# Performance work log

Measured on AMD Instinct MI355X. Metric: run time of the kernel, lower is better.

The kernel has to match this reference:

```python
import jax, jax.numpy as jnp
import numpy as np

N_NODES = 50000
N_EDGES = 500000
IN_CH = 128
HID = 32
HEADS = 4
OUT_CH = 64
NEG_SLOPE = 0.2


def setup_inputs() -> dict:
    key = jax.random.key(0)
    ks = jax.random.split(key, 12)
    s = 0.1  # weight init scale
    x = jax.random.normal(ks[0], (N_NODES, IN_CH), jnp.float32)
    edge_index = jax.random.randint(ks[1], (2, N_EDGES), 0, N_NODES)
    # conv1: GATv2Conv(IN_CH, HID, heads=HEADS)
    W1l = jax.random.normal(ks[2], (IN_CH, HEADS * HID), jnp.float32) * s  # lin_l (source)
    W1r = jax.random.normal(ks[3], (IN_CH, HEADS * HID), jnp.float32) * s  # lin_r (target)
    att1 = jax.random.normal(ks[4], (HEADS, HID), jnp.float32) * s
    b1 = jnp.zeros((HEADS * HID,), jnp.float32)
    # conv2: GATv2Conv(HEADS*HID, OUT_CH, heads=1, concat=False)
    W2l = jax.random.normal(ks[5], (HEADS * HID, OUT_CH), jnp.float32) * s
    W2r = jax.random.normal(ks[6], (HEADS * HID, OUT_CH), jnp.float32) * s
    att2 = jax.random.normal(ks[7], (1, OUT_CH), jnp.float32) * s
    b2 = jnp.zeros((OUT_CH,), jnp.float32)
    return {"x": x, "edge_index": edge_index, "W1l": W1l, "W1r": W1r,
            "att1": att1, "b1": b1, "W2l": W2l, "W2r": W2r, "att2": att2, "b2": b2}


def gatv2_conv(x, src, dst, Wl, Wr, att, heads, ch, num_nodes):
    """GATv2Conv message passing. Returns [N, heads, ch] (pre-bias, pre-concat)."""
    xl = (x @ Wl).reshape(num_nodes, heads, ch)  # source transform
    xr = (x @ Wr).reshape(num_nodes, heads, ch)  # target transform
    xl_e = xl[src]                               # [E, H, C] gathered source feats
    m = jax.nn.leaky_relu(xl_e + xr[dst], NEG_SLOPE)
    score = jnp.einsum('ehc,hc->eh', m, att)     # [E, H]
    # segment softmax over incoming edges per destination node
    smax = jax.ops.segment_max(score, dst, num_segments=num_nodes)
    smax = jnp.where(jnp.isfinite(smax), smax, 0.0)
    p = jnp.exp(score - smax[dst])
    denom = jax.ops.segment_sum(p, dst, num_segments=num_nodes)
    alpha = p / (denom[dst] + 1e-16)
    out = jax.ops.segment_sum(alpha[:, :, None] * xl_e, dst, num_segments=num_nodes)
    return out


def reference(x, edge_index, W1l, W1r, att1, b1, W2l, W2r, att2, b2):
    n = x.shape[0]
    loop = jnp.arange(n, dtype=edge_index.dtype)
    src = jnp.concatenate([edge_index[0], loop])  # add self-loops (PyG default)
    dst = jnp.concatenate([edge_index[1], loop])
    # dropout(p=0.6) is identity in eval mode
    h = gatv2_conv(x, src, dst, W1l, W1r, att1, HEADS, HID, n)
    h = h.reshape(n, HEADS * HID) + b1            # concat=True
    h = jax.nn.elu(h)
    o = gatv2_conv(h, src, dst, W2l, W2r, att2, 1, OUT_CH, n)  # [N, 1, OUT]
    o = o + b2                                     # concat=False, heads=1 -> mean == identity
    return o[:, 0, :]
```

## Files before the change

kernel.cpp:

```cpp
#include <hip/hip_runtime.h>
#include <hip/hip_bf16.h>
#include <math.h>

#define N_NODESC 50000
#define N_EDGESC 500000
#define E_TOT    (N_EDGESC + N_NODESC)
#define IN_CH 128
#define HID 32
#define HEADS 4
#define HC (HEADS*HID)
#define OUT_CH 64
#define NEG_SLOPE 0.2f
#define NB_SCAN 196
#define N_STRIPS (N_NODESC/16)

typedef unsigned short u16;
typedef __attribute__((ext_vector_type(8))) short short8;
typedef __attribute__((ext_vector_type(4))) float floatx4;

__device__ __forceinline__ u16 f2bf(float f){
  unsigned u = __float_as_uint(f);
  return (u16)((u + 0x7FFFu + ((u >> 16) & 1u)) >> 16);
}
__device__ __forceinline__ float bf2f(u16 b){ return __uint_as_float(((unsigned)b) << 16); }
__device__ __forceinline__ float bflo(unsigned q){ return __uint_as_float(q << 16); }
__device__ __forceinline__ float bfhi(unsigned q){ return __uint_as_float(q & 0xFFFF0000u); }
__device__ __forceinline__ float lrelu(float v){ return (v > 0.f) ? v : NEG_SLOPE*v; }

__device__ __forceinline__ void edge_sd(const int* __restrict__ ei, int e, int& s, int& d){
  if (e < N_EDGESC){ s = ei[e]; d = ei[N_EDGESC + e]; }
  else { s = e - N_EDGESC; d = s; }
}

__global__ void k_zero_deg(int* __restrict__ deg){
  int i = blockIdx.x*blockDim.x + threadIdx.x;
  if (i < N_NODESC) deg[i] = 0;
}

__global__ void k_hist(const int* __restrict__ ei, int* __restrict__ deg){
  int e = blockIdx.x*blockDim.x + threadIdx.x;
  if (e >= E_TOT) return;
  int s, d; edge_sd(ei, e, s, d);
  atomicAdd(&deg[d], 1);
}

__global__ void k_scan_a(const int* __restrict__ deg, int* __restrict__ rs,
                         int* __restrict__ bsum){
  __shared__ int sh[256];
  int i = blockIdx.x*256 + threadIdx.x;
  int v = (i < N_NODESC) ? deg[i] : 0;
  sh[threadIdx.x] = v;
  __syncthreads();
  for (int off=1; off<256; off<<=1){
    int t = (threadIdx.x >= off) ? sh[threadIdx.x-off] : 0;
    __syncthreads();
    sh[threadIdx.x] += t;
    __syncthreads();
  }
  if (i < N_NODESC) rs[i] = sh[threadIdx.x] - v;
  if (threadIdx.x == 255) bsum[blockIdx.x] = sh[255];
}

__global__ void k_scan_b(int* __restrict__ bsum){
  __shared__ int sh[256];
  int v = (threadIdx.x < NB_SCAN) ? bsum[threadIdx.x] : 0;
  sh[threadIdx.x] = v;
  __syncthreads();
  for (int off=1; off<256; off<<=1){
    int t = (threadIdx.x >= off) ? sh[threadIdx.x-off] : 0;
    __syncthreads();
    sh[threadIdx.x] += t;
    __syncthreads();
  }
  if (threadIdx.x < NB_SCAN) bsum[threadIdx.x] = sh[threadIdx.x] - v;
}

__global__ void k_scan_c(int* __restrict__ rs, const int* __restrict__ bsum,
                         int* __restrict__ cursor){
  int i = blockIdx.x*256 + threadIdx.x;
  if (i >= N_NODESC) return;
  int v = rs[i] + bsum[blockIdx.x];
  rs[i] = v;
  cursor[i] = v;
}

__global__ void k_fill(const int* __restrict__ ei, int* __restrict__ cursor,
                       int* __restrict__ csrc){
  int e = blockIdx.x*blockDim.x + threadIdx.x;
  if (e >= E_TOT) return;
  int s, d; edge_sd(ei, e, s, d);
  int pos = atomicAdd(&cursor[d], 1);
  csrc[pos] = s;
}

__global__ void k_split(const float* __restrict__ X, u16* __restrict__ hi,
                        u16* __restrict__ lo, int total4){
  int i = blockIdx.x*blockDim.x + threadIdx.x;
  if (i >= total4) return;
  float4 v = ((const float4*)X)[i];
  ushort4 h, l;
  h.x = f2bf(v.x); l.x = f2bf(v.x - bf2f(h.x));
  h.y = f2bf(v.y); l.y = f2bf(v.y - bf2f(h.y));
  h.z = f2bf(v.z); l.z = f2bf(v.z - bf2f(h.z));
  h.w = f2bf(v.w); l.w = f2bf(v.w - bf2f(h.w));
  ((ushort4*)hi)[i] = h;
  ((ushort4*)lo)[i] = l;
}

__global__ void k_prep_all(const float* __restrict__ W1l, const float* __restrict__ W1r,
                           const float* __restrict__ W2l, const float* __restrict__ W2r,
                           u16* __restrict__ w1lh, u16* __restrict__ w1rh,
                           u16* __restrict__ w2lh, u16* __restrict__ w2rh){
  int b = blockIdx.x;
  const float* W; u16 *Th; int N, base;
  if (b < 8)      { W=W1l; Th=w1lh; N=HC;     base=b;    }
  else if (b < 16){ W=W1r; Th=w1rh; N=HC;     base=b-8;  }
  else if (b < 20){ W=W2l; Th=w2lh; N=OUT_CH; base=b-16; }
  else            { W=W2r; Th=w2rh; N=OUT_CH; base=b-20; }
  int tid = base*256 + threadIdx.x;
  int lane = tid & 63;
  int t = (tid >> 6) & 3;
  int c = tid >> 8;
  int k0 = t*32 + (lane>>4)*8;
  int n  = c*16 + (lane&15);
  #pragma unroll
  for (int j=0;j<8;j++){
    Th[(size_t)tid*8 + j] = f2bf(W[(size_t)(k0+j)*N + n]);
  }
}

template<int NCW, int SPB>
__launch_bounds__(256, 2)
__global__ void k_gemm_regB(const u16* __restrict__ Ahi, const u16* __restrict__ Alo,
                            const u16* __restrict__ BlT, const u16* __restrict__ BrT,
                            u16* __restrict__ Olb, float* __restrict__ Or){
  constexpr int NLD = 2*NCW*16;
  int wave = threadIdx.x >> 6, lane = threadIdx.x & 63;
  int m = lane & 15, quad = lane >> 4;
  bool isl = (wave < 2);
  int ctbase = (isl ? wave : wave - 2) * NCW;
  const u16* __restrict__ BT = isl ? BlT : BrT;

  short8 breg[NCW][4];
  #pragma unroll
  for (int c=0;c<NCW;c++)
    #pragma unroll
    for (int t=0;t<4;t++)
      breg[c][t] = *(const short8*)(BT + ((size_t)(((ctbase+c)*4 + t)*64) + lane)*8);

  int strip0 = blockIdx.x * SPB;
  short8 ah[2][4], al[2][4];

  {
    const u16* p1 = Ahi + (size_t)(strip0*16 + m)*128 + quad*8;
    const u16* p2 = Alo + (size_t)(strip0*16 + m)*128 + quad*8;
    #pragma unroll
    for (int t=0;t<4;t++){
      ah[0][t] = *(const short8*)(p1 + t*32);
      al[0][t] = *(const short8*)(p2 + t*32);
    }
  }

  #pragma unroll
  for (int i=0;i<SPB;i++){
    int s = strip0 + i;
    if (s >= N_STRIPS) break;
    if (i+1 < SPB && s+1 < N_STRIPS){
      const u16* p1 = Ahi + (size_t)((s+1)*16 + m)*128 + quad*8;
      const u16* p2 = Alo + (size_t)((s+1)*16 + m)*128 + quad*8;
      #pragma unroll
      for (int t=0;t<4;t++){
        ah[(i+1)&1][t] = *(const short8*)(p1 + t*32);
        al[(i+1)&1][t] = *(const short8*)(p2 + t*32);
      }
    }
    const int b = i&1;
    floatx4 acc[NCW];
    #pragma unroll
    for (int c=0;c<NCW;c++) acc[c] = (floatx4){0.f,0.f,0.f,0.f};
    #pragma unroll
    for (int t=0;t<4;t++){
      #pragma unroll
      for (int c=0;c<NCW;c++){
        acc[c] = __builtin_amdgcn_mfma_f32_16x16x32_bf16(ah[b][t], breg[c][t], acc[c], 0,0,0);
        acc[c] = __builtin_amdgcn_mfma_f32_16x16x32_bf16(al[b][t], breg[c][t], acc[c], 0,0,0);
      }
    }
    int row0 = s*16;
    if (isl){
      #pragma unroll
      for (int c=0;c<NCW;c++)
        #pragma unroll
        for (int r=0;r<4;r++)
          Olb[(size_t)(row0 + quad*4 + r)*NLD + (ctbase+c)*16 + m] = f2bf(acc[c][r]);
    } else {
      #pragma unroll
      for (int c=0;c<NCW;c++)
        #pragma unroll
        for (int r=0;r<4;r++)
          Or[(size_t)(row0 + quad*4 + r)*NLD + (ctbase+c)*16 + m] = acc[c][r];
    }
  }
}

__global__ void k_fused1(const int* __restrict__ rs, const int* __restrict__ deg,
                         const int* __restrict__ csrc, const u16* __restrict__ xlb,
                         const float* __restrict__ xr, const float* __restrict__ att,
                         const float* __restrict__ b1,
                         u16* __restrict__ Hhi, u16* __restrict__ Hlo){
  int wave = threadIdx.x >> 6;
  int lane = threadIdx.x & 63;
  int d = blockIdx.x*4 + wave;
  if (d >= N_NODESC) return;

  float2 xrv = ((const float2*)(xr + (size_t)d*HC))[lane];
  float2 atv = ((const float2*)att)[lane];
  float2 bv  = ((const float2*)b1)[lane];

  int start = rs[d];
  int degd  = deg[d];
  const unsigned* __restrict__ xt = (const unsigned*)xlb;

  float lden = 0.f;
  float2 acc = {0.f, 0.f};

  int i = 0;
  int s0=0,s1=0,s2=0,s3=0;
  if (degd >= 4){
    s0 = csrc[start+0]; s1 = csrc[start+1]; s2 = csrc[start+2]; s3 = csrc[start+3];
  }
  for (; i + 4 <= degd; ){
    int t0=s0, t1=s1, t2=s2, t3=s3;
    int ni = i + 4;
    if (ni + 4 <= degd){
      s0 = csrc[start+ni+0]; s1 = csrc[start+ni+1];
      s2 = csrc[start+ni+2]; s3 = csrc[start+ni+3];
    }
    unsigned q0 = xt[(size_t)t0*64 + lane];
    unsigned q1 = xt[(size_t)t1*64 + lane];
    unsigned q2 = xt[(size_t)t2*64 + lane];
    unsigned q3 = xt[(size_t)t3*64 + lane];

    float sc0 = lrelu(bflo(q0)+xrv.x)*atv.x + lrelu(bfhi(q0)+xrv.y)*atv.y;
    float sc1 = lrelu(bflo(q1)+xrv.x)*atv.x + lrelu(bfhi(q1)+xrv.y)*atv.y;
    float sc2 = lrelu(bflo(q2)+xrv.x)*atv.x + lrelu(bfhi(q2)+xrv.y)*atv.y;
    float sc3 = lrelu(bflo(q3)+xrv.x)*atv.x + lrelu(bfhi(q3)+xrv.y)*atv.y;
    #pragma unroll
    for (int off=1; off<16; off<<=1){
      sc0 += __shfl_xor(sc0, off);
      sc1 += __shfl_xor(sc1, off);
      sc2 += __shfl_xor(sc2, off);
      sc3 += __shfl_xor(sc3, off);
    }
    float p0 = __expf(sc0), p1 = __expf(sc1), p2 = __expf(sc2), p3 = __expf(sc3);
    lden += (p0+p1) + (p2+p3);
    acc.x += p0*bflo(q0) + p1*bflo(q1) + p2*bflo(q2) + p3*bflo(q3);
    acc.y += p0*bfhi(q0) + p1*bfhi(q1) + p2*bfhi(q2) + p3*bfhi(q3);
    i = ni;
  }
  for (; i < degd; i++){
    int s = csrc[start+i];
    unsigned q = xt[(size_t)s*64 + lane];
    float sc = lrelu(bflo(q)+xrv.x)*atv.x + lrelu(bfhi(q)+xrv.y)*atv.y;
    #pragma unroll
    for (int off=1; off<16; off<<=1) sc += __shfl_xor(sc, off);
    float p = __expf(sc);
    lden += p;
    acc.x += p*bflo(q);
    acc.y += p*bfhi(q);
  }

  float inv = 1.f / (lden + 1e-16f);
  float ox = acc.x*inv + bv.x;
  float oy = acc.y*inv + bv.y;
  ox = (ox > 0.f) ? ox : (__expf(ox) - 1.f);
  oy = (oy > 0.f) ? oy : (__expf(oy) - 1.f);

  u16 hx = f2bf(ox), hy = f2bf(oy);
  ushort2 hh; hh.x = hx; hh.y = hy;
  ushort2 hl; hl.x = f2bf(ox - bf2f(hx)); hl.y = f2bf(oy - bf2f(hy));
  ((ushort2*)(Hhi + (size_t)d*HC))[lane] = hh;
  ((ushort2*)(Hlo + (size_t)d*HC))[lane] = hl;
}

__global__ void k_fused2(const int* __restrict__ rs, const int* __restrict__ deg,
                         const int* __restrict__ csrc, const u16* __restrict__ xlb,
                         const float* __restrict__ xr, const float* __restrict__ att,
                         const float* __restrict__ b2, float* __restrict__ out){
  int wave = threadIdx.x >> 6;
  int lane = threadIdx.x & 63;
  int d = blockIdx.x*4 + wave;
  if (d >= N_NODESC) return;

  float xrv = xr[(size_t)d*OUT_CH + lane];
  float atv = att[lane];
  float bv  = b2[lane];

  int start = rs[d];
  int degd  = deg[d];

  float lden = 0.f, acc = 0.f;

  int i = 0;
  int s0=0,s1=0,s2=0,s3=0;
  if (degd >= 4){
    s0 = csrc[start+0]; s1 = csrc[start+1]; s2 = csrc[start+2]; s3 = csrc[start+3];
  }
  for (; i + 4 <= degd; ){
    int t0=s0, t1=s1, t2=s2, t3=s3;
    int ni = i + 4;
    if (ni + 4 <= degd){
      s0 = csrc[start+ni+0]; s1 = csrc[start+ni+1];
      s2 = csrc[start+ni+2]; s3 = csrc[start+ni+3];
    }
    float x0 = bf2f(xlb[(size_t)t0*OUT_CH + lane]);
    float x1 = bf2f(xlb[(size_t)t1*OUT_CH + lane]);
    float x2 = bf2f(xlb[(size_t)t2*OUT_CH + lane]);
    float x3 = bf2f(xlb[(size_t)t3*OUT_CH + lane]);

    float sc0 = lrelu(x0+xrv)*atv;
    float sc1 = lrelu(x1+xrv)*atv;
    float sc2 = lrelu(x2+xrv)*atv;
    float sc3 = lrelu(x3+xrv)*atv;
    #pragma unroll
    for (int off=1; off<64; off<<=1){
      sc0 += __shfl_xor(sc0, off);
      sc1 += __shfl_xor(sc1, off);
      sc2 += __shfl_xor(sc2, off);
      sc3 += __shfl_xor(sc3, off);
    }
    float p0 = __expf(sc0), p1 = __expf(sc1), p2 = __expf(sc2), p3 = __expf(sc3);
    lden += (p0+p1) + (p2+p3);
    acc += p0*x0 + p1*x1 + p2*x2 + p3*x3;
    i = ni;
  }
  for (; i < degd; i++){
    int s = csrc[start+i];
    float xv = bf2f(xlb[(size_t)s*OUT_CH + lane]);
    float sc = lrelu(xv+xrv)*atv;
    #pragma unroll
    for (int off=1; off<64; off<<=1) sc += __shfl_xor(sc, off);
    float p = __expf(sc);
    lden += p;
    acc  += p*xv;
  }
  out[(size_t)d*OUT_CH + lane] = acc / (lden + 1e-16f) + bv;
}

extern "C" void kernel_launch(void* const* d_in, const int* in_sizes, int n_in,
                              void* d_out, int out_size, void* d_ws, size_t ws_size,
                              hipStream_t stream) {
  const float* x    = (const float*)d_in[0];
  const int*   ei   = (const int*)d_in[1];
  const float* W1l  = (const float*)d_in[2];
  const float* W1r  = (const float*)d_in[3];
  const float* att1 = (const float*)d_in[4];
  const float* b1   = (const float*)d_in[5];
  const float* W2l  = (const float*)d_in[6];
  const float* W2r  = (const float*)d_in[7];
  const float* att2 = (const float*)d_in[8];
  const float* b2   = (const float*)d_in[9];
  float* out = (float*)d_out;

  float* ws = (float*)d_ws;
  size_t off = 0;
  float* xr1 = ws + off; off += (size_t)N_NODESC*HC;
  float* xr2 = ws + off; off += (size_t)N_NODESC*OUT_CH;
  u16* xl1b = (u16*)(ws + off); off += (size_t)N_NODESC*HC/2;
  u16* xl2b = (u16*)(ws + off); off += (size_t)N_NODESC*OUT_CH/2;
  u16* xhi = (u16*)(ws + off); off += (size_t)N_NODESC*HC/2;
  u16* xlo = (u16*)(ws + off); off += (size_t)N_NODESC*HC/2;
  u16* hhi = (u16*)(ws + off); off += (size_t)N_NODESC*HC/2;
  u16* hlo = (u16*)(ws + off); off += (size_t)N_NODESC*HC/2;
  u16* w1lh = (u16*)(ws + off); off += IN_CH*HC/2;
  u16* w1rh = (u16*)(ws + off); off += IN_CH*HC/2;
  u16* w2lh = (u16*)(ws + off); off += HC*OUT_CH/2;
  u16* w2rh = (u16*)(ws + off); off += HC*OUT_CH/2;
  int* deg    = (int*)(ws + off); off += N_NODESC;
  int* rs     = (int*)(ws + off); off += N_NODESC;
  int* cursor = (int*)(ws + off); off += N_NODESC;
  int* bsum   = (int*)(ws + off); off += 256;
  int* csrc   = (int*)(ws + off); off += E_TOT;

  k_zero_deg<<<(N_NODESC+255)/256, 256, 0, stream>>>(deg);
  k_hist<<<(E_TOT+255)/256, 256, 0, stream>>>(ei, deg);
  k_scan_a<<<NB_SCAN, 256, 0, stream>>>(deg, rs, bsum);
  k_scan_b<<<1, 256, 0, stream>>>(bsum);
  k_scan_c<<<NB_SCAN, 256, 0, stream>>>(rs, bsum, cursor);
  k_fill<<<(E_TOT+255)/256, 256, 0, stream>>>(ei, cursor, csrc);

  k_split<<<((N_NODESC*HC/4)+255)/256, 256, 0, stream>>>(x, xhi, xlo, N_NODESC*HC/4);
  k_prep_all<<<24, 256, 0, stream>>>(W1l, W1r, W2l, W2r, w1lh, w1rh, w2lh, w2rh);

  const int NB_G = (N_STRIPS + 3)/4;
  k_gemm_regB<4,4><<<NB_G, 256, 0, stream>>>(xhi, xlo, w1lh, w1rh, xl1b, xr1);
  k_fused1<<<(N_NODESC+3)/4, 256, 0, stream>>>(rs, deg, csrc, xl1b, xr1, att1, b1, hhi, hlo);

  k_gemm_regB<2,4><<<NB_G, 256, 0, stream>>>(hhi, hlo, w2lh, w2rh, xl2b, xr2);
  k_fused2<<<(N_NODESC+3)/4, 256, 0, stream>>>(rs, deg, csrc, xl2b, xr2, att2, b2, out);
}
```

Measured before the change: 271.6 us.

## Split each wave into four edge groups with vectorized feature loads in GAT aggregation

Both aggregation kernels now divide the 64-lane wave into four 16-lane groups, and each group handles a different incoming edge at the same time. Each lane loads 8 (layer 1) or 4 (layer 2) bf16 features with a single vector load. This shortens the per-edge shuffle reductions, from 4 steps to 2 in layer 1 and from 6 to 4 in layer 2, and it issues fewer, wider gathers. The cost is a cross-group reduction of the accumulators at the end, and lanes in the last partial group of 4 edges do wasted work, with their contributions masked out.

Result: faster. 262.7 us (-3.3%).

```diff
diff --git a/kernel.cpp b/kernel.cpp
--- a/kernel.cpp
+++ b/kernel.cpp
@@ -16,6 +16,8 @@
 
 typedef unsigned short u16;
 typedef __attribute__((ext_vector_type(8))) short short8;
+typedef __attribute__((ext_vector_type(8))) unsigned short ushort8v;
+typedef __attribute__((ext_vector_type(4))) unsigned short ushort4v;
 typedef __attribute__((ext_vector_type(4))) float floatx4;
 
 __device__ __forceinline__ u16 f2bf(float f){
@@ -23,8 +25,6 @@
   return (u16)((u + 0x7FFFu + ((u >> 16) & 1u)) >> 16);
 }
 __device__ __forceinline__ float bf2f(u16 b){ return __uint_as_float(((unsigned)b) << 16); }
-__device__ __forceinline__ float bflo(unsigned q){ return __uint_as_float(q << 16); }
-__device__ __forceinline__ float bfhi(unsigned q){ return __uint_as_float(q & 0xFFFF0000u); }
 __device__ __forceinline__ float lrelu(float v){ return (v > 0.f) ? v : NEG_SLOPE*v; }
 
 __device__ __forceinline__ void edge_sd(const int* __restrict__ ei, int e, int& s, int& d){
@@ -212,75 +212,65 @@
   int lane = threadIdx.x & 63;
   int d = blockIdx.x*4 + wave;
   if (d >= N_NODESC) return;
-
-  float2 xrv = ((const float2*)(xr + (size_t)d*HC))[lane];
-  float2 atv = ((const float2*)att)[lane];
-  float2 bv  = ((const float2*)b1)[lane];
-
-  int start = rs[d];
-  int degd  = deg[d];
-  const unsigned* __restrict__ xt = (const unsigned*)xlb;
-
-  float lden = 0.f;
-  float2 acc = {0.f, 0.f};
-
-  int i = 0;
-  int s0=0,s1=0,s2=0,s3=0;
-  if (degd >= 4){
-    s0 = csrc[start+0]; s1 = csrc[start+1]; s2 = csrc[start+2]; s3 = csrc[start+3];
-  }
-  for (; i + 4 <= degd; ){
-    int t0=s0, t1=s1, t2=s2, t3=s3;
-    int ni = i + 4;
-    if (ni + 4 <= degd){
-      s0 = csrc[start+ni+0]; s1 = csrc[start+ni+1];
-      s2 = csrc[start+ni+2]; s3 = csrc[start+ni+3];
-    }
-    unsigned q0 = xt[(size_t)t0*64 + lane];
-    unsigned q1 = xt[(size_t)t1*64 + lane];
-    unsigned q2 = xt[(size_t)t2*64 + lane];
-    unsigned q3 = xt[(size_t)t3*64 + lane];
-
-    float sc0 = lrelu(bflo(q0)+xrv.x)*atv.x + lrelu(bfhi(q0)+xrv.y)*atv.y;
-    float sc1 = lrelu(bflo(q1)+xrv.x)*atv.x + lrelu(bfhi(q1)+xrv.y)*atv.y;
-    float sc2 = lrelu(bflo(q2)+xrv.x)*atv.x + lrelu(bfhi(q2)+xrv.y)*atv.y;
-    float sc3 = lrelu(bflo(q3)+xrv.x)*atv.x + lrelu(bfhi(q3)+xrv.y)*atv.y;
-    #pragma unroll
-    for (int off=1; off<16; off<<=1){
-      sc0 += __shfl_xor(sc0, off);
-      sc1 += __shfl_xor(sc1, off);
-      sc2 += __shfl_xor(sc2, off);
-      sc3 += __shfl_xor(sc3, off);
-    }
-    float p0 = __expf(sc0), p1 = __expf(sc1), p2 = __expf(sc2), p3 = __expf(sc3);
-    lden += (p0+p1) + (p2+p3);
-    acc.x += p0*bflo(q0) + p1*bflo(q1) + p2*bflo(q2) + p3*bflo(q3);
-    acc.y += p0*bfhi(q0) + p1*bfhi(q1) + p2*bfhi(q2) + p3*bfhi(q3);
-    i = ni;
-  }
-  for (; i < degd; i++){
-    int s = csrc[start+i];
-    unsigned q = xt[(size_t)s*64 + lane];
-    float sc = lrelu(bflo(q)+xrv.x)*atv.x + lrelu(bfhi(q)+xrv.y)*atv.y;
-    #pragma unroll
-    for (int off=1; off<16; off<<=1) sc += __shfl_xor(sc, off);
-    float p = __expf(sc);
-    lden += p;
-    acc.x += p*bflo(q);
-    acc.y += p*bfhi(q);
-  }
-
-  float inv = 1.f / (lden + 1e-16f);
-  float ox = acc.x*inv + bv.x;
-  float oy = acc.y*inv + bv.y;
-  ox = (ox > 0.f) ? ox : (__expf(ox) - 1.f);
-  oy = (oy > 0.f) ? oy : (__expf(oy) - 1.f);
-
-  u16 hx = f2bf(ox), hy = f2bf(oy);
-  ushort2 hh; hh.x = hx; hh.y = hy;
-  ushort2 hl; hl.x = f2bf(ox - bf2f(hx)); hl.y = f2bf(oy - bf2f(hy));
-  ((ushort2*)(Hhi + (size_t)d*HC))[lane] = hh;
-  ((ushort2*)(Hlo + (size_t)d*HC))[lane] = hl;
+  int g = lane >> 4;
+  int l = lane & 15;
+
+  float xrv[8], atv[8], bv[8];
+  const float* xrp = xr + (size_t)d*HC + 8*l;
+  #pragma unroll
+  for (int j=0;j<8;j++){ xrv[j] = xrp[j]; atv[j] = att[8*l+j]; bv[j] = b1[8*l+j]; }
+
+  int start = rs[d], degd = deg[d];
+
+  float acc[8];
+  #pragma unroll
+  for (int j=0;j<8;j++) acc[j] = 0.f;
+  float den = 0.f;
+
+  int e0 = g;
+  int s_cur = csrc[start + ((e0 < degd) ? e0 : 0)];
+  for (int i = 0; i < degd; i += 4){
+    bool valid = (i + g < degd);
+    int s = s_cur;
+    int en = i + 4 + g;
+    s_cur = csrc[start + ((en < degd) ? en : 0)];
+    ushort8v q = *(const ushort8v*)(xlb + (size_t)s*HC + 8*l);
+    float xv[8];
+    float sc = 0.f;
+    #pragma unroll
+    for (int j=0;j<8;j++){
+      xv[j] = bf2f(q[j]);
+      sc += lrelu(xv[j] + xrv[j]) * atv[j];
+    }
+    sc += __shfl_xor(sc, 1);
+    sc += __shfl_xor(sc, 2);
+    float p = valid ? __expf(sc) : 0.f;
+    den += p;
+    #pragma unroll
+    for (int j=0;j<8;j++) acc[j] += p * xv[j];
+  }
+  #pragma unroll
+  for (int j=0;j<8;j++){
+    acc[j] += __shfl_xor(acc[j], 16);
+    acc[j] += __shfl_xor(acc[j], 32);
+  }
+  den += __shfl_xor(den, 16);
+  den += __shfl_xor(den, 32);
+
+  if (g == 0){
+    float inv = 1.f / (den + 1e-16f);
+    ushort8v oh, ol;
+    #pragma unroll
+    for (int j=0;j<8;j++){
+      float o = acc[j]*inv + bv[j];
+      o = (o > 0.f) ? o : (__expf(o) - 1.f);
+      u16 h = f2bf(o);
+      oh[j] = h;
+      ol[j] = f2bf(o - bf2f(h));
+    }
+    *(ushort8v*)(Hhi + (size_t)d*HC + 8*l) = oh;
+    *(ushort8v*)(Hlo + (size_t)d*HC + 8*l) = ol;
+  }
 }
 
 __global__ void k_fused2(const int* __restrict__ rs, const int* __restrict__ deg,
@@ -291,60 +281,60 @@
   int lane = threadIdx.x & 63;
   int d = blockIdx.x*4 + wave;
   if (d >= N_NODESC) return;
-
-  float xrv = xr[(size_t)d*OUT_CH + lane];
-  float atv = att[lane];
-  float bv  = b2[lane];
-
-  int start = rs[d];
-  int degd  = deg[d];
-
-  float lden = 0.f, acc = 0.f;
-
-  int i = 0;
-  int s0=0,s1=0,s2=0,s3=0;
-  if (degd >= 4){
-    s0 = csrc[start+0]; s1 = csrc[start+1]; s2 = csrc[start+2]; s3 = csrc[start+3];
-  }
-  for (; i + 4 <= degd; ){
-    int t0=s0, t1=s1, t2=s2, t3=s3;
-    int ni = i + 4;
-    if (ni + 4 <= degd){
-      s0 = csrc[start+ni+0]; s1 = csrc[start+ni+1];
-      s2 = csrc[start+ni+2]; s3 = csrc[start+ni+3];
-    }
-    float x0 = bf2f(xlb[(size_t)t0*OUT_CH + lane]);
-    float x1 = bf2f(xlb[(size_t)t1*OUT_CH + lane]);
-    float x2 = bf2f(xlb[(size_t)t2*OUT_CH + lane]);
-    float x3 = bf2f(xlb[(size_t)t3*OUT_CH + lane]);
-
-    float sc0 = lrelu(x0+xrv)*atv;
-    float sc1 = lrelu(x1+xrv)*atv;
-    float sc2 = lrelu(x2+xrv)*atv;
-    float sc3 = lrelu(x3+xrv)*atv;
-    #pragma unroll
-    for (int off=1; off<64; off<<=1){
-      sc0 += __shfl_xor(sc0, off);
-      sc1 += __shfl_xor(sc1, off);
-      sc2 += __shfl_xor(sc2, off);
-      sc3 += __shfl_xor(sc3, off);
-    }
-    float p0 = __expf(sc0), p1 = __expf(sc1), p2 = __expf(sc2), p3 = __expf(sc3);
-    lden += (p0+p1) + (p2+p3);
-    acc += p0*x0 + p1*x1 + p2*x2 + p3*x3;
-    i = ni;
-  }
-  for (; i < degd; i++){
-    int s = csrc[start+i];
-    float xv = bf2f(xlb[(size_t)s*OUT_CH + lane]);
-    float sc = lrelu(xv+xrv)*atv;
-    #pragma unroll
-    for (int off=1; off<64; off<<=1) sc += __shfl_xor(sc, off);
-    float p = __expf(sc);
-    lden += p;
-    acc  += p*xv;
-  }
-  out[(size_t)d*OUT_CH + lane] = acc / (lden + 1e-16f) + bv;
+  int g = lane >> 4;
+  int l = lane & 15;
+
+  float xrv[4], atv[4], bv[4];
+  const float* xrp = xr + (size_t)d*OUT_CH + 4*l;
+  #pragma unroll
+  for (int j=0;j<4;j++){ xrv[j] = xrp[j]; atv[j] = att[4*l+j]; bv[j] = b2[4*l+j]; }
+
+  int start = rs[d], degd = deg[d];
+
+  float acc[4] = {0.f,0.f,0.f,0.f};
+  float den = 0.f;
+
+  int e0 = g;
+  int s_cur = csrc[start + ((e0 < degd) ? e0 : 0)];
+  for (int i = 0; i < degd; i += 4){
+    bool valid = (i + g < degd);
+    int s = s_cur;
+    int en = i + 4 + g;
+    s_cur = csrc[start + ((en < degd) ? en : 0)];
+    ushort4v q = *(const ushort4v*)(xlb + (size_t)s*OUT_CH + 4*l);
+    float xv[4];
+    float sc = 0.f;
+    #pragma unroll
+    for (int j=0;j<4;j++){
+      xv[j] = bf2f(q[j]);
+      sc += lrelu(xv[j] + xrv[j]) * atv[j];
+    }
+    sc += __shfl_xor(sc, 1);
+    sc += __shfl_xor(sc, 2);
+    sc += __shfl_xor(sc, 4);
+    sc += __shfl_xor(sc, 8);
+    float p = valid ? __expf(sc) : 0.f;
+    den += p;
+    #pragma unroll
+    for (int j=0;j<4;j++) acc[j] += p * xv[j];
+  }
+  #pragma unroll
+  for (int j=0;j<4;j++){
+    acc[j] += __shfl_xor(acc[j], 16);
+    acc[j] += __shfl_xor(acc[j], 32);
+  }
+  den += __shfl_xor(den, 16);
+  den += __shfl_xor(den, 32);
+
+  if (g == 0){
+    float inv = 1.f / (den + 1e-16f);
+    float4 o;
+    o.x = acc[0]*inv + bv[0];
+    o.y = acc[1]*inv + bv[1];
+    o.z = acc[2]*inv + bv[2];
+    o.w = acc[3]*inv + bv[3];
+    *(float4*)(out + (size_t)d*OUT_CH + 4*l) = o;
+  }
 }
 
 extern "C" void kernel_launch(void* const* d_in, const int* in_sizes, int n_in,
```
